# Kernel optimization log

Hardware: AMD Instinct MI355X
Metric: run time of the kernel (lower is better)

## Reference

```python
import jax, jax.numpy as jnp
import numpy as np

WIN = 7
SHIFT = 3
HEADS = 6
EPS = 1e-5


def _rel_pos_index(ws):
    coords = np.stack(np.meshgrid(np.arange(ws), np.arange(ws), indexing='ij')).reshape(2, -1)
    rel = (coords[:, :, None] - coords[:, None, :]).transpose(1, 2, 0)  # (N, N, 2)
    rel[..., 0] += ws - 1
    rel[..., 1] += ws - 1
    rel[..., 0] *= 2 * ws - 1
    return jnp.asarray(rel.sum(-1).reshape(-1))  # (N*N,)


def _attn_mask(H, W, ws, ss):
    img = np.zeros((H, W))
    sl = (slice(0, -ws), slice(-ws, -ss), slice(-ss, None))
    cnt = 0
    for hs in sl:
        for wss in sl:
            img[hs, wss] = cnt
            cnt += 1
    mw = img.reshape(H // ws, ws, W // ws, ws).transpose(0, 2, 1, 3).reshape(-1, ws * ws)
    am = mw[:, None, :] - mw[:, :, None]  # (nw, N, N): mw[j]-mw[i]
    return jnp.asarray(np.where(am != 0, -1e9, 0.0).astype(np.float32))


def _layernorm(x, g, b):
    mu = x.mean(-1, keepdims=True)
    var = ((x - mu) ** 2).mean(-1, keepdims=True)
    return (x - mu) * jax.lax.rsqrt(var + EPS) * g + b


def setup_inputs() -> dict:
    key = jax.random.key(0)
    ks = jax.random.split(key, 6)
    B, H, W, C = 4, 224, 224, 192
    return {
        'x': jax.random.normal(ks[0], (B, H * W, C), jnp.float32),
        'norm1_g': jnp.ones((C,), jnp.float32),
        'norm1_b': jnp.zeros((C,), jnp.float32),
        'qkv_w': jax.random.normal(ks[1], (C, 3 * C), jnp.float32) * 0.02,
        'qkv_b': jnp.zeros((3 * C,), jnp.float32),
        'rpb_table': jax.random.normal(ks[2], ((2 * WIN - 1) ** 2, HEADS), jnp.float32) * 0.02,
        'proj_w': jax.random.normal(ks[3], (C, C), jnp.float32) * 0.02,
        'proj_b': jnp.zeros((C,), jnp.float32),
        'norm2_g': jnp.ones((C,), jnp.float32),
        'norm2_b': jnp.zeros((C,), jnp.float32),
        'fc1_w': jax.random.normal(ks[4], (C, 4 * C), jnp.float32) * 0.02,
        'fc1_b': jnp.zeros((4 * C,), jnp.float32),
        'fc2_w': jax.random.normal(ks[5], (4 * C, C), jnp.float32) * 0.02,
        'fc2_b': jnp.zeros((C,), jnp.float32),
        'h': 224,
        'w': 224,
    }


def reference(x, norm1_g, norm1_b, qkv_w, qkv_b, rpb_table, proj_w, proj_b,
              norm2_g, norm2_b, fc1_w, fc1_b, fc2_w, fc2_b, h, w):
    B, L, C = x.shape
    ch = C // HEADS
    N = WIN * WIN
    nh, nw = h // WIN, w // WIN
    rel_idx = _rel_pos_index(WIN)
    mask = _attn_mask(h, w, WIN, SHIFT)  # (nh*nw, N, N)

    shortcut = x
    xn = _layernorm(x, norm1_g, norm1_b).reshape(B, h, w, C)
    xs = jnp.roll(xn, (-SHIFT, -SHIFT), axis=(1, 2))
    # window partition -> (B*nh*nw, N, C)
    xw = xs.reshape(B, nh, WIN, nw, WIN, C).transpose(0, 1, 3, 2, 4, 5).reshape(B * nh * nw, N, C)

    qkv = (xw @ qkv_w + qkv_b).reshape(-1, N, 3, HEADS, ch).transpose(2, 0, 3, 1, 4)
    q, k, v = qkv[0], qkv[1], qkv[2]  # (NW, HEADS, N, ch)
    scale = ch ** -0.5
    attn = jnp.einsum('whic,whjc->whij', q * scale, k)
    bias = rpb_table[rel_idx].reshape(N, N, HEADS).transpose(2, 0, 1)  # (HEADS, N, N)
    attn = attn + bias[None]
    attn = attn.reshape(B, nh * nw, HEADS, N, N) + mask[None, :, None]
    attn = jax.nn.softmax(attn, axis=-1).reshape(B * nh * nw, HEADS, N, N)

    out = jnp.einsum('whij,whjc->whic', attn, v).transpose(0, 2, 1, 3).reshape(-1, N, C)
    out = out @ proj_w + proj_b
    # window reverse + roll back
    out = out.reshape(B, nh, nw, WIN, WIN, C).transpose(0, 1, 3, 2, 4, 5).reshape(B, h, w, C)
    out = jnp.roll(out, (SHIFT, SHIFT), axis=(1, 2)).reshape(B, L, C)

    x = shortcut + out
    xn2 = _layernorm(x, norm2_g, norm2_b)
    hid = jax.nn.gelu(xn2 @ fc1_w + fc1_b, approximate=False)
    return x + (hid @ fc2_w + fc2_b)
```

## Files before the change

### kernel.cpp

```cpp
#include <hip/hip_runtime.h>
#include <stdint.h>

#define MB    50176
#define WINB  1024
#define CDIM  192

typedef __attribute__((ext_vector_type(8))) short bf16x8;
typedef __attribute__((ext_vector_type(4))) float f32x4;

__device__ __forceinline__ float wsum(float v){
  #pragma unroll
  for (int m=32;m>=1;m>>=1) v += __shfl_xor(v,m,64);
  return v;
}
__device__ __forceinline__ float bfbits2f(uint32_t h){
  union{uint32_t u; float f;} x; x.u = h<<16; return x.f;
}
__device__ __forceinline__ uint16_t f2bfbits(float f){
  union{float ff; uint32_t u;} x; x.ff = f;
  return (uint16_t)((x.u + 0x7FFFu + ((x.u>>16)&1u)) >> 16);
}
__device__ __forceinline__ void gload16(const void* g, void* l){
  __builtin_amdgcn_global_load_lds(
      (const __attribute__((address_space(1))) uint32_t*)g,
      (__attribute__((address_space(3))) uint32_t*)l, 16, 0, 0);
}

__global__ __launch_bounds__(256) void wconv_kernel(
    const float* __restrict__ W, uint16_t* __restrict__ WT, int K, int N){
  int idx = blockIdx.x*256 + threadIdx.x;
  if (idx >= K*N) return;
  int k = idx / N, n = idx - k*N;
  WT[(size_t)n*K + k] = f2bfbits(W[idx]);
}

__global__ __launch_bounds__(256) void btbl_kernel(
    const float* __restrict__ rpb, float* __restrict__ tbl){
  int idx = blockIdx.x*256 + threadIdx.x;
  if (idx >= 4*6*64*64) return;
  int j = idx & 63, i = (idx>>6) & 63;
  int hd = (idx>>12) % 6, cls = idx >> 12; cls /= 6;
  float v = -1e9f;
  if (i < 49 && j < 49){
    int dh = i/7 - j/7, dw = i%7 - j%7;
    v = rpb[((dh+6)*13 + (dw+6))*6 + hd];
    int cH = cls>>1, cW = cls&1;
    int li = (cH ? (i/7 < 4 ? 1 : 2) : 0)*3 + (cW ? (i%7 < 4 ? 1 : 2) : 0);
    int lj = (cH ? (j/7 < 4 ? 1 : 2) : 0)*3 + (cW ? (j%7 < 4 ? 1 : 2) : 0);
    if (li != lj) v = -1e9f;
  }
  tbl[idx] = v;
}

template<bool GATHER>
__global__ __launch_bounds__(256) void ln_kernel(
    const float* __restrict__ src, const float* __restrict__ g,
    const float* __restrict__ bt, uint16_t* __restrict__ dst){
  int wid  = (int)((blockIdx.x*256u + threadIdx.x) >> 6);
  int lane = threadIdx.x & 63;
  int sidx;
  if (GATHER){
    int widx = wid/49, tpos = wid - widx*49;
    int wh = widx>>5, ww = widx&31;
    int th = tpos/7, tw = tpos - th*7;
    int h = wh*7+th+3; if (h>=224) h-=224;
    int w = ww*7+tw+3; if (w>=224) w-=224;
    sidx = h*224 + w;
  } else {
    sidx = wid;
  }
  const float* s = src + (size_t)sidx*CDIM;
  float v0=s[lane], v1=s[lane+64], v2=s[lane+128];
  float mu  = wsum(v0+v1+v2) * (1.f/192.f);
  float var = wsum(v0*v0+v1*v1+v2*v2)*(1.f/192.f) - mu*mu;
  float rs  = rsqrtf(var + 1e-5f);
  uint16_t* d = dst + (size_t)wid*CDIM;
  d[lane]     = f2bfbits((v0-mu)*rs*g[lane]     + bt[lane]);
  d[lane+64]  = f2bfbits((v1-mu)*rs*g[lane+64]  + bt[lane+64]);
  d[lane+128] = f2bfbits((v2-mu)*rs*g[lane+128] + bt[lane+128]);
}

enum { EPI_QKV=0, EPI_PROJ=1, EPI_FC1=2, EPI_FC2=3 };

template<int EPI, int K, int NN>
__global__ __launch_bounds__(256) void mgemm(
    const uint16_t* __restrict__ A, const uint16_t* __restrict__ WT,
    const float* __restrict__ bias, void* __restrict__ outp,
    const float* __restrict__ resid){
  __shared__ __attribute__((aligned(16))) char As[128*128];
  __shared__ __attribute__((aligned(16))) char Bs[64*128];
  const int tid  = threadIdx.x;
  const int lane = tid & 63;
  const int wid  = tid >> 6;
  const int brow = blockIdx.y * 128;
  const int bcol = blockIdx.x * 64;

  f32x4 acc[4][2];
  #pragma unroll
  for (int m=0;m<4;m++)
    #pragma unroll
    for (int n=0;n<2;n++) acc[m][n] = (f32x4){0.f,0.f,0.f,0.f};

  const int srow = lane >> 3;
  const int sg   = (lane & 7) ^ srow;
  const int wm = wid >> 1, wn = wid & 1;
  const int lrow16 = lane & 15, lkh = lane >> 4;

  for (int k0 = 0; k0 < K; k0 += 64){
    #pragma unroll
    for (int c = 0; c < 4; c++){
      int ch = wid*4 + c;
      const uint16_t* g = A + (size_t)(brow + ch*8 + srow)*K + k0 + sg*8;
      gload16(g, As + ch*1024);
    }
    #pragma unroll
    for (int c = 0; c < 2; c++){
      int ch = wid*2 + c;
      const uint16_t* g = WT + (size_t)(bcol + ch*8 + srow)*K + k0 + sg*8;
      gload16(g, Bs + ch*1024);
    }
    __syncthreads();

    bf16x8 af[4][2], bfr[2][2];
    #pragma unroll
    for (int m=0;m<4;m++)
      #pragma unroll
      for (int ks=0;ks<2;ks++){
        int arow = wm*64 + m*16 + lrow16;
        int g0 = ks*4 + lkh;
        af[m][ks] = *(const bf16x8*)(As + arow*128 + ((g0 ^ (arow&7))<<4));
      }
    #pragma unroll
    for (int n=0;n<2;n++)
      #pragma unroll
      for (int ks=0;ks<2;ks++){
        int brn = wn*32 + n*16 + lrow16;
        int g0 = ks*4 + lkh;
        bfr[n][ks] = *(const bf16x8*)(Bs + brn*128 + ((g0 ^ (brn&7))<<4));
      }
    #pragma unroll
    for (int m=0;m<4;m++)
      #pragma unroll
      for (int n=0;n<2;n++)
        #pragma unroll
        for (int ks=0;ks<2;ks++)
          acc[m][n] = __builtin_amdgcn_mfma_f32_16x16x32_bf16(
              af[m][ks], bfr[n][ks], acc[m][n], 0, 0, 0);
    __syncthreads();
  }

  float bi[2];
  #pragma unroll
  for (int n=0;n<2;n++) bi[n] = bias[bcol + wn*32 + n*16 + lrow16];
  #pragma unroll
  for (int m=0;m<4;m++){
    #pragma unroll
    for (int j=0;j<4;j++){
      int r = brow + wm*64 + m*16 + lkh*4 + j;
      if constexpr (EPI==EPI_QKV || EPI==EPI_FC1){
        #pragma unroll
        for (int n=0;n<2;n++){
          float v = acc[m][n][j] + bi[n];
          if constexpr (EPI==EPI_FC1)
            v = 0.5f*v*(1.f + erff(v*0.70710678118654752f));
          ((uint16_t*)outp)[(size_t)r*NN + bcol + wn*32 + n*16 + lrow16] = f2bfbits(v);
        }
      } else if constexpr (EPI==EPI_PROJ){
        int widx = r/49, tpos = r - widx*49;
        int wh = widx>>5, ww = widx&31;
        int th = tpos/7, tw = tpos - th*7;
        int h = wh*7+th+3; if (h>=224) h-=224;
        int w = ww*7+tw+3; if (w>=224) w-=224;
        size_t pr = ((size_t)h*224 + w)*CDIM;
        #pragma unroll
        for (int n=0;n<2;n++){
          size_t p = pr + bcol + wn*32 + n*16 + lrow16;
          ((float*)outp)[p] = acc[m][n][j] + bi[n] + resid[p];
        }
      } else {
        size_t pr = (size_t)r*NN;
        #pragma unroll
        for (int n=0;n<2;n++){
          size_t p = pr + bcol + wn*32 + n*16 + lrow16;
          ((float*)outp)[p] = acc[m][n][j] + bi[n] + resid[p];
        }
      }
    }
  }
}

__global__ __launch_bounds__(64) void attn_kernel(
    const uint16_t* __restrict__ qkv, const float* __restrict__ btbl,
    uint16_t* __restrict__ attnout){
  const int bid  = blockIdx.x;
  const int widx = bid/6, hd = bid - widx*6;
  const int lane = threadIdx.x;
  const int r16 = lane & 15, t4 = lane >> 4;
  __shared__ uint16_t Vt[32][72];
  __shared__ uint16_t Pl[4][16][72];

  #pragma unroll
  for (int e=lane; e<32*16; e+=64){ Vt[e>>4][48 + (e&15)] = 0; }
  for (int ch = lane; ch < 196; ch += 64){
    int j = ch >> 2, c0 = (ch&3)*8;
    const uint16_t* src = qkv + ((size_t)widx*49 + j)*576 + hd*32 + 384 + c0;
    uint4 v = *(const uint4*)src;
    uint32_t u[4] = {v.x, v.y, v.z, v.w};
    #pragma unroll
    for (int q=0;q<8;q++) Vt[c0+q][j] = (uint16_t)(u[q>>1] >> ((q&1)*16));
  }

  bf16x8 kf[4], qf[4];
  #pragma unroll
  for (int jt=0;jt<4;jt++)
    kf[jt] = *(const bf16x8*)(qkv + ((size_t)widx*49 + jt*16 + r16)*576 + hd*32 + 192 + t4*8);
  #pragma unroll
  for (int it=0;it<4;it++)
    qf[it] = *(const bf16x8*)(qkv + ((size_t)widx*49 + it*16 + r16)*576 + hd*32 + t4*8);
  f32x4 acc[4][4];
  #pragma unroll
  for (int jt=0;jt<4;jt++)
    #pragma unroll
    for (int it=0;it<4;it++){
      acc[jt][it] = (f32x4){0.f,0.f,0.f,0.f};
      acc[jt][it] = __builtin_amdgcn_mfma_f32_16x16x32_bf16(kf[jt], qf[it], acc[jt][it], 0,0,0);
    }

  const int wh = widx>>5, ww = widx&31;
  const int cls = ((wh==31)<<1) | (ww==31);
  const float* tb = btbl + ((size_t)(cls*6 + hd) << 12);
  const float scale = 0.17677669529663689f;
  #pragma unroll
  for (int it=0;it<4;it++){
    int i = it*16 + r16;
    float s[4][4];
    float m = -3.4e38f;
    #pragma unroll
    for (int jt=0;jt<4;jt++){
      float4 bv = *(const float4*)(tb + i*64 + jt*16 + t4*4);
      float bb[4] = {bv.x, bv.y, bv.z, bv.w};
      #pragma unroll
      for (int r=0;r<4;r++){
        s[jt][r] = acc[jt][it][r]*scale + bb[r];
        m = fmaxf(m, s[jt][r]);
      }
    }
    m = fmaxf(m, __shfl_xor(m, 16, 64));
    m = fmaxf(m, __shfl_xor(m, 32, 64));
    float sum = 0.f;
    #pragma unroll
    for (int jt=0;jt<4;jt++)
      #pragma unroll
      for (int r=0;r<4;r++){
        s[jt][r] = __expf(s[jt][r] - m);
        sum += s[jt][r];
      }
    sum += __shfl_xor(sum, 16, 64);
    sum += __shfl_xor(sum, 32, 64);
    float inv = 1.f / sum;
    #pragma unroll
    for (int jt=0;jt<4;jt++){
      uint32_t lo = (uint32_t)f2bfbits(s[jt][0]*inv) | ((uint32_t)f2bfbits(s[jt][1]*inv) << 16);
      uint32_t hi = (uint32_t)f2bfbits(s[jt][2]*inv) | ((uint32_t)f2bfbits(s[jt][3]*inv) << 16);
      *(uint2*)&Pl[it][r16][jt*16 + t4*4] = make_uint2(lo, hi);
    }
  }
  __syncthreads();

  bf16x8 bv[2][2];
  #pragma unroll
  for (int ct=0;ct<2;ct++)
    #pragma unroll
    for (int ks=0;ks<2;ks++)
      bv[ct][ks] = *(const bf16x8*)&Vt[ct*16 + r16][ks*32 + t4*8];
  #pragma unroll
  for (int it=0;it<4;it++){
    f32x4 o[2];
    o[0] = (f32x4){0.f,0.f,0.f,0.f};
    o[1] = (f32x4){0.f,0.f,0.f,0.f};
    #pragma unroll
    for (int ks=0;ks<2;ks++){
      bf16x8 pa = *(const bf16x8*)&Pl[it][r16][ks*32 + t4*8];
      #pragma unroll
      for (int ct=0;ct<2;ct++)
        o[ct] = __builtin_amdgcn_mfma_f32_16x16x32_bf16(pa, bv[ct][ks], o[ct], 0,0,0);
    }
    #pragma unroll
    for (int r=0;r<4;r++){
      int i = it*16 + t4*4 + r;
      if (i < 49){
        size_t base = ((size_t)widx*49 + i)*CDIM + hd*32;
        attnout[base + r16]      = f2bfbits(o[0][r]);
        attnout[base + 16 + r16] = f2bfbits(o[1][r]);
      }
    }
  }
}

extern "C" void kernel_launch(void* const* d_in, const int* in_sizes, int n_in,
                              void* d_out, int out_size, void* d_ws, size_t ws_size,
                              hipStream_t stream) {
  const float* x       = (const float*)d_in[0];
  const float* n1g     = (const float*)d_in[1];
  const float* n1b     = (const float*)d_in[2];
  const float* qkv_w   = (const float*)d_in[3];
  const float* qkv_b   = (const float*)d_in[4];
  const float* rpb     = (const float*)d_in[5];
  const float* proj_w  = (const float*)d_in[6];
  const float* proj_b  = (const float*)d_in[7];
  const float* n2g     = (const float*)d_in[8];
  const float* n2b     = (const float*)d_in[9];
  const float* fc1_w   = (const float*)d_in[10];
  const float* fc1_b   = (const float*)d_in[11];
  const float* fc2_w   = (const float*)d_in[12];
  const float* fc2_b   = (const float*)d_in[13];
  float* out = (float*)d_out;

  char* ws = (char*)d_ws;
  uint16_t* Abuf = (uint16_t*)ws;
  uint16_t* Bq   = (uint16_t*)(ws + (size_t)MB*CDIM*2);
  char*     wbase = ws + (size_t)MB*CDIM*2 + (size_t)MB*768*2;
  uint16_t* qkvW = (uint16_t*)wbase;
  uint16_t* prjW = (uint16_t*)(wbase + 221184);
  uint16_t* fc1W = (uint16_t*)(wbase + 221184 + 73728);
  uint16_t* fc2W = (uint16_t*)(wbase + 221184 + 73728 + 294912);
  float*    btbl = (float*)(wbase + 221184 + 73728 + 294912 + 294912);

  wconv_kernel<<<(192*576+255)/256, 256, 0, stream>>>(qkv_w,  qkvW, 192, 576);
  wconv_kernel<<<(192*192+255)/256, 256, 0, stream>>>(proj_w, prjW, 192, 192);
  wconv_kernel<<<(192*768+255)/256, 256, 0, stream>>>(fc1_w,  fc1W, 192, 768);
  wconv_kernel<<<(768*192+255)/256, 256, 0, stream>>>(fc2_w,  fc2W, 768, 192);
  btbl_kernel<<<(4*6*64*64+255)/256, 256, 0, stream>>>(rpb, btbl);

  for (int b=0;b<4;b++){
    const float* xb = x   + (size_t)b*MB*CDIM;
    float*      ob  = out + (size_t)b*MB*CDIM;
    ln_kernel<true><<<MB/4, 256, 0, stream>>>(xb, n1g, n1b, Abuf);
    mgemm<EPI_QKV, 192, 576>
        <<<dim3(9, MB/128), 256, 0, stream>>>(Abuf, qkvW, qkv_b, (void*)Bq, nullptr);
    attn_kernel<<<WINB*6, 64, 0, stream>>>(Bq, btbl, Abuf);
    mgemm<EPI_PROJ, 192, 192>
        <<<dim3(3, MB/128), 256, 0, stream>>>(Abuf, prjW, proj_b, (void*)ob, xb);
  }
  for (int b=0;b<4;b++){
    float* ob = out + (size_t)b*MB*CDIM;
    ln_kernel<false><<<MB/4, 256, 0, stream>>>(ob, n2g, n2b, Abuf);
    mgemm<EPI_FC1, 192, 768>
        <<<dim3(12, MB/128), 256, 0, stream>>>(Abuf, fc1W, fc1_b, (void*)Bq, nullptr);
    mgemm<EPI_FC2, 768, 192>
        <<<dim3(3, MB/128), 256, 0, stream>>>(Bq, fc2W, fc2_b, (void*)ob, ob);
  }
}
```

Before: 835.0 us.

## Fuse projection with LayerNorm2, batch all images per launch, merge prep kernels

```diff
diff --git a/kernel.cpp b/kernel.cpp
--- a/kernel.cpp
+++ b/kernel.cpp
@@ -2,7 +2,6 @@
 #include <stdint.h>
 
 #define MB    50176
-#define WINB  1024
 #define CDIM  192
 
 typedef __attribute__((ext_vector_type(8))) short bf16x8;
@@ -25,21 +24,33 @@
       (const __attribute__((address_space(1))) uint32_t*)g,
       (__attribute__((address_space(3))) uint32_t*)l, 16, 0, 0);
 }
-
-__global__ __launch_bounds__(256) void wconv_kernel(
-    const float* __restrict__ W, uint16_t* __restrict__ WT, int K, int N){
+__device__ __forceinline__ size_t row2tok(int r_g){
+  int widx = r_g/49, tpos = r_g - widx*49;
+  int b = widx>>10, rem = widx&1023;
+  int h = (rem>>5)*7 + tpos/7 + 3; if (h>=224) h-=224;
+  int w = (rem&31)*7 + (tpos - (tpos/7)*7) + 3; if (w>=224) w-=224;
+  return (size_t)b*MB + (size_t)h*224 + w;
+}
+
+__global__ __launch_bounds__(256) void prep_kernel(
+    const float* __restrict__ qkv_w, const float* __restrict__ proj_w,
+    const float* __restrict__ fc1_w, const float* __restrict__ fc2_w,
+    const float* __restrict__ rpb,
+    uint16_t* __restrict__ qkvW, uint16_t* __restrict__ prjW,
+    uint16_t* __restrict__ fc1W, uint16_t* __restrict__ fc2W,
+    float* __restrict__ btbl){
   int idx = blockIdx.x*256 + threadIdx.x;
-  if (idx >= K*N) return;
-  int k = idx / N, n = idx - k*N;
-  WT[(size_t)n*K + k] = f2bfbits(W[idx]);
-}
-
-__global__ __launch_bounds__(256) void btbl_kernel(
-    const float* __restrict__ rpb, float* __restrict__ tbl){
-  int idx = blockIdx.x*256 + threadIdx.x;
-  if (idx >= 4*6*64*64) return;
+  if (idx < 110592){ int k=idx/576, n=idx-k*576; qkvW[n*192+k]=f2bfbits(qkv_w[idx]); return; }
+  idx -= 110592;
+  if (idx < 36864){ int k=idx/192, n=idx-k*192; prjW[n*192+k]=f2bfbits(proj_w[idx]); return; }
+  idx -= 36864;
+  if (idx < 147456){ int k=idx/768, n=idx-k*768; fc1W[n*192+k]=f2bfbits(fc1_w[idx]); return; }
+  idx -= 147456;
+  if (idx < 147456){ int k=idx/192, n=idx-k*192; fc2W[n*768+k]=f2bfbits(fc2_w[idx]); return; }
+  idx -= 147456;
+  if (idx >= 98304) return;
   int j = idx & 63, i = (idx>>6) & 63;
-  int hd = (idx>>12) % 6, cls = idx >> 12; cls /= 6;
+  int hd = (idx>>12) % 6, cls = (idx>>12)/6;
   float v = -1e9f;
   if (i < 49 && j < 49){
     int dh = i/7 - j/7, dw = i%7 - j%7;
@@ -49,44 +60,33 @@
     int lj = (cH ? (j/7 < 4 ? 1 : 2) : 0)*3 + (cW ? (j%7 < 4 ? 1 : 2) : 0);
     if (li != lj) v = -1e9f;
   }
-  tbl[idx] = v;
-}
-
-template<bool GATHER>
-__global__ __launch_bounds__(256) void ln_kernel(
-    const float* __restrict__ src, const float* __restrict__ g,
-    const float* __restrict__ bt, uint16_t* __restrict__ dst){
-  int wid  = (int)((blockIdx.x*256u + threadIdx.x) >> 6);
-  int lane = threadIdx.x & 63;
-  int sidx;
-  if (GATHER){
-    int widx = wid/49, tpos = wid - widx*49;
-    int wh = widx>>5, ww = widx&31;
-    int th = tpos/7, tw = tpos - th*7;
-    int h = wh*7+th+3; if (h>=224) h-=224;
-    int w = ww*7+tw+3; if (w>=224) w-=224;
-    sidx = h*224 + w;
-  } else {
-    sidx = wid;
-  }
-  const float* s = src + (size_t)sidx*CDIM;
+  btbl[idx] = v;
+}
+
+__global__ __launch_bounds__(256) void ln1_kernel(
+    const float* __restrict__ x, const float* __restrict__ g,
+    const float* __restrict__ bt, uint16_t* __restrict__ dst, int row0){
+  int wid_l = (int)((blockIdx.x*256u + threadIdx.x) >> 6);
+  int lane  = threadIdx.x & 63;
+  size_t sidx = row2tok(row0 + wid_l);
+  const float* s = x + sidx*CDIM;
   float v0=s[lane], v1=s[lane+64], v2=s[lane+128];
   float mu  = wsum(v0+v1+v2) * (1.f/192.f);
   float var = wsum(v0*v0+v1*v1+v2*v2)*(1.f/192.f) - mu*mu;
   float rs  = rsqrtf(var + 1e-5f);
-  uint16_t* d = dst + (size_t)wid*CDIM;
+  uint16_t* d = dst + (size_t)wid_l*CDIM;
   d[lane]     = f2bfbits((v0-mu)*rs*g[lane]     + bt[lane]);
   d[lane+64]  = f2bfbits((v1-mu)*rs*g[lane+64]  + bt[lane+64]);
   d[lane+128] = f2bfbits((v2-mu)*rs*g[lane+128] + bt[lane+128]);
 }
 
-enum { EPI_QKV=0, EPI_PROJ=1, EPI_FC1=2, EPI_FC2=3 };
+enum { EPI_QKV=0, EPI_FC1=2, EPI_FC2=3 };
 
 template<int EPI, int K, int NN>
 __global__ __launch_bounds__(256) void mgemm(
     const uint16_t* __restrict__ A, const uint16_t* __restrict__ WT,
     const float* __restrict__ bias, void* __restrict__ outp,
-    const float* __restrict__ resid){
+    const float* __restrict__ resid, int row0){
   __shared__ __attribute__((aligned(16))) char As[128*128];
   __shared__ __attribute__((aligned(16))) char Bs[64*128];
   const int tid  = threadIdx.x;
@@ -110,14 +110,12 @@
     #pragma unroll
     for (int c = 0; c < 4; c++){
       int ch = wid*4 + c;
-      const uint16_t* g = A + (size_t)(brow + ch*8 + srow)*K + k0 + sg*8;
-      gload16(g, As + ch*1024);
+      gload16(A + (size_t)(brow + ch*8 + srow)*K + k0 + sg*8, As + ch*1024);
     }
     #pragma unroll
     for (int c = 0; c < 2; c++){
       int ch = wid*2 + c;
-      const uint16_t* g = WT + (size_t)(bcol + ch*8 + srow)*K + k0 + sg*8;
-      gload16(g, Bs + ch*1024);
+      gload16(WT + (size_t)(bcol + ch*8 + srow)*K + k0 + sg*8, Bs + ch*1024);
     }
     __syncthreads();
 
@@ -127,16 +125,14 @@
       #pragma unroll
       for (int ks=0;ks<2;ks++){
         int arow = wm*64 + m*16 + lrow16;
-        int g0 = ks*4 + lkh;
-        af[m][ks] = *(const bf16x8*)(As + arow*128 + ((g0 ^ (arow&7))<<4));
+        af[m][ks] = *(const bf16x8*)(As + arow*128 + (((ks*4+lkh) ^ (arow&7))<<4));
       }
     #pragma unroll
     for (int n=0;n<2;n++)
       #pragma unroll
       for (int ks=0;ks<2;ks++){
         int brn = wn*32 + n*16 + lrow16;
-        int g0 = ks*4 + lkh;
-        bfr[n][ks] = *(const bf16x8*)(Bs + brn*128 + ((g0 ^ (brn&7))<<4));
+        bfr[n][ks] = *(const bf16x8*)(Bs + brn*128 + (((ks*4+lkh) ^ (brn&7))<<4));
       }
     #pragma unroll
     for (int m=0;m<4;m++)
@@ -165,25 +161,120 @@
             v = 0.5f*v*(1.f + erff(v*0.70710678118654752f));
           ((uint16_t*)outp)[(size_t)r*NN + bcol + wn*32 + n*16 + lrow16] = f2bfbits(v);
         }
-      } else if constexpr (EPI==EPI_PROJ){
-        int widx = r/49, tpos = r - widx*49;
-        int wh = widx>>5, ww = widx&31;
-        int th = tpos/7, tw = tpos - th*7;
-        int h = wh*7+th+3; if (h>=224) h-=224;
-        int w = ww*7+tw+3; if (w>=224) w-=224;
-        size_t pr = ((size_t)h*224 + w)*CDIM;
+      } else {
+        size_t pr = row2tok(row0 + r)*CDIM;
         #pragma unroll
         for (int n=0;n<2;n++){
           size_t p = pr + bcol + wn*32 + n*16 + lrow16;
           ((float*)outp)[p] = acc[m][n][j] + bi[n] + resid[p];
         }
-      } else {
-        size_t pr = (size_t)r*NN;
+      }
+    }
+  }
+}
+
+__global__ __launch_bounds__(384) void proj_ln2(
+    const uint16_t* __restrict__ A, const uint16_t* __restrict__ WT,
+    const float* __restrict__ pbias, const float* __restrict__ x,
+    const float* __restrict__ g2, const float* __restrict__ b2,
+    float* __restrict__ xout, uint16_t* __restrict__ ln2out, int row0){
+  __shared__ __attribute__((aligned(16))) char As[128*128];
+  __shared__ __attribute__((aligned(16))) char Bs[192*128];
+  __shared__ float stats[3][128][2];
+  const int tid  = threadIdx.x;
+  const int lane = tid & 63;
+  const int wid  = tid >> 6;
+  const int wm = wid >> 2, wn3 = wid & 3;
+  const int pm = wid / 3, pn = wid - pm*3;
+  const int brow = blockIdx.x * 128;
+  const int srow = lane >> 3;
+  const int sg   = (lane & 7) ^ srow;
+  const int lrow16 = lane & 15, lkh = lane >> 4;
+  (void)wm; (void)wn3;
+
+  f32x4 acc[4][4];
+  #pragma unroll
+  for (int m=0;m<4;m++)
+    #pragma unroll
+    for (int n=0;n<4;n++) acc[m][n] = (f32x4){0.f,0.f,0.f,0.f};
+
+  for (int k0 = 0; k0 < 192; k0 += 64){
+    for (int ch = wid; ch < 16; ch += 6)
+      gload16(A + (size_t)(brow + ch*8 + srow)*192 + k0 + sg*8, As + ch*1024);
+    for (int ch = wid; ch < 24; ch += 6)
+      gload16(WT + (size_t)(ch*8 + srow)*192 + k0 + sg*8, Bs + ch*1024);
+    __syncthreads();
+
+    bf16x8 af[4][2], bfr[4][2];
+    #pragma unroll
+    for (int m=0;m<4;m++)
+      #pragma unroll
+      for (int ks=0;ks<2;ks++){
+        int arow = pm*64 + m*16 + lrow16;
+        af[m][ks] = *(const bf16x8*)(As + arow*128 + (((ks*4+lkh) ^ (arow&7))<<4));
+      }
+    #pragma unroll
+    for (int n=0;n<4;n++)
+      #pragma unroll
+      for (int ks=0;ks<2;ks++){
+        int brn = pn*64 + n*16 + lrow16;
+        bfr[n][ks] = *(const bf16x8*)(Bs + brn*128 + (((ks*4+lkh) ^ (brn&7))<<4));
+      }
+    #pragma unroll
+    for (int m=0;m<4;m++)
+      #pragma unroll
+      for (int n=0;n<4;n++)
         #pragma unroll
-        for (int n=0;n<2;n++){
-          size_t p = pr + bcol + wn*32 + n*16 + lrow16;
-          ((float*)outp)[p] = acc[m][n][j] + bi[n] + resid[p];
-        }
+        for (int ks=0;ks<2;ks++)
+          acc[m][n] = __builtin_amdgcn_mfma_f32_16x16x32_bf16(
+              af[m][ks], bfr[n][ks], acc[m][n], 0, 0, 0);
+    __syncthreads();
+  }
+
+  float bi[4], g2v[4], b2v[4];
+  #pragma unroll
+  for (int n=0;n<4;n++){
+    int c = pn*64 + n*16 + lrow16;
+    bi[n] = pbias[c]; g2v[n] = g2[c]; b2v[n] = b2[c];
+  }
+  #pragma unroll
+  for (int m=0;m<4;m++){
+    #pragma unroll
+    for (int j=0;j<4;j++){
+      int r = pm*64 + m*16 + lkh*4 + j;
+      size_t pr = row2tok(row0 + brow + r)*CDIM;
+      float s1 = 0.f, s2 = 0.f;
+      #pragma unroll
+      for (int n=0;n<4;n++){
+        int c = pn*64 + n*16 + lrow16;
+        float y = acc[m][n][j] + bi[n] + x[pr + c];
+        acc[m][n][j] = y;
+        xout[pr + c] = y;
+        s1 += y; s2 = fmaf(y, y, s2);
+      }
+      #pragma unroll
+      for (int mk=1; mk<16; mk<<=1){
+        s1 += __shfl_xor(s1, mk, 64);
+        s2 += __shfl_xor(s2, mk, 64);
+      }
+      if (lrow16 == 0){ stats[pn][r][0] = s1; stats[pn][r][1] = s2; }
+    }
+  }
+  __syncthreads();
+  #pragma unroll
+  for (int m=0;m<4;m++){
+    #pragma unroll
+    for (int j=0;j<4;j++){
+      int r = pm*64 + m*16 + lkh*4 + j;
+      float s1 = stats[0][r][0] + stats[1][r][0] + stats[2][r][0];
+      float s2 = stats[0][r][1] + stats[1][r][1] + stats[2][r][1];
+      float mu = s1*(1.f/192.f);
+      float rs = rsqrtf(s2*(1.f/192.f) - mu*mu + 1e-5f);
+      size_t pr = (size_t)(brow + r)*CDIM;
+      #pragma unroll
+      for (int n=0;n<4;n++){
+        int c = pn*64 + n*16 + lrow16;
+        ln2out[pr + c] = f2bfbits((acc[m][n][j]-mu)*rs*g2v[n] + b2v[n]);
       }
     }
   }
@@ -191,13 +282,13 @@
 
 __global__ __launch_bounds__(64) void attn_kernel(
     const uint16_t* __restrict__ qkv, const float* __restrict__ btbl,
-    uint16_t* __restrict__ attnout){
+    uint16_t* __restrict__ attnout, int win0){
   const int bid  = blockIdx.x;
   const int widx = bid/6, hd = bid - widx*6;
   const int lane = threadIdx.x;
   const int r16 = lane & 15, t4 = lane >> 4;
   __shared__ uint16_t Vt[32][72];
-  __shared__ uint16_t Pl[4][16][72];
+  __shared__ uint16_t Pl[16][72];
 
   #pragma unroll
   for (int e=lane; e<32*16; e+=64){ Vt[e>>4][48 + (e&15)] = 0; }
@@ -225,11 +316,20 @@
       acc[jt][it] = (f32x4){0.f,0.f,0.f,0.f};
       acc[jt][it] = __builtin_amdgcn_mfma_f32_16x16x32_bf16(kf[jt], qf[it], acc[jt][it], 0,0,0);
     }
-
-  const int wh = widx>>5, ww = widx&31;
-  const int cls = ((wh==31)<<1) | (ww==31);
+  __syncthreads();
+
+  const int gw = win0 + widx;
+  const int cls = ((((gw&1023)>>5)==31)<<1) | ((gw&31)==31);
   const float* tb = btbl + ((size_t)(cls*6 + hd) << 12);
   const float scale = 0.17677669529663689f;
+
+  bf16x8 bv[2][2];
+  #pragma unroll
+  for (int ct=0;ct<2;ct++)
+    #pragma unroll
+    for (int ks=0;ks<2;ks++)
+      bv[ct][ks] = *(const bf16x8*)&Vt[ct*16 + r16][ks*32 + t4*8];
+
   #pragma unroll
   for (int it=0;it<4;it++){
     int i = it*16 + r16;
@@ -237,8 +337,8 @@
     float m = -3.4e38f;
     #pragma unroll
     for (int jt=0;jt<4;jt++){
-      float4 bv = *(const float4*)(tb + i*64 + jt*16 + t4*4);
-      float bb[4] = {bv.x, bv.y, bv.z, bv.w};
+      float4 bvv = *(const float4*)(tb + i*64 + jt*16 + t4*4);
+      float bb[4] = {bvv.x, bvv.y, bvv.z, bvv.w};
       #pragma unroll
       for (int r=0;r<4;r++){
         s[jt][r] = acc[jt][it][r]*scale + bb[r];
@@ -262,34 +362,25 @@
     for (int jt=0;jt<4;jt++){
       uint32_t lo = (uint32_t)f2bfbits(s[jt][0]*inv) | ((uint32_t)f2bfbits(s[jt][1]*inv) << 16);
       uint32_t hi = (uint32_t)f2bfbits(s[jt][2]*inv) | ((uint32_t)f2bfbits(s[jt][3]*inv) << 16);
-      *(uint2*)&Pl[it][r16][jt*16 + t4*4] = make_uint2(lo, hi);
-    }
-  }
-  __syncthreads();
-
-  bf16x8 bv[2][2];
-  #pragma unroll
-  for (int ct=0;ct<2;ct++)
-    #pragma unroll
-    for (int ks=0;ks<2;ks++)
-      bv[ct][ks] = *(const bf16x8*)&Vt[ct*16 + r16][ks*32 + t4*8];
-  #pragma unroll
-  for (int it=0;it<4;it++){
+      *(uint2*)&Pl[r16][jt*16 + t4*4] = make_uint2(lo, hi);
+    }
+    __syncthreads();
+
     f32x4 o[2];
     o[0] = (f32x4){0.f,0.f,0.f,0.f};
     o[1] = (f32x4){0.f,0.f,0.f,0.f};
     #pragma unroll
     for (int ks=0;ks<2;ks++){
-      bf16x8 pa = *(const bf16x8*)&Pl[it][r16][ks*32 + t4*8];
+      bf16x8 pa = *(const bf16x8*)&Pl[r16][ks*32 + t4*8];
       #pragma unroll
       for (int ct=0;ct<2;ct++)
         o[ct] = __builtin_amdgcn_mfma_f32_16x16x32_bf16(pa, bv[ct][ks], o[ct], 0,0,0);
     }
     #pragma unroll
     for (int r=0;r<4;r++){
-      int i = it*16 + t4*4 + r;
-      if (i < 49){
-        size_t base = ((size_t)widx*49 + i)*CDIM + hd*32;
+      int i2 = it*16 + t4*4 + r;
+      if (i2 < 49){
+        size_t base = ((size_t)widx*49 + i2)*CDIM + hd*32;
         attnout[base + r16]      = f2bfbits(o[0][r]);
         attnout[base + 16 + r16] = f2bfbits(o[1][r]);
       }
@@ -316,38 +407,37 @@
   const float* fc2_b   = (const float*)d_in[13];
   float* out = (float*)d_out;
 
+  const size_t TBL = 221184 + 73728 + 294912 + 294912 + 393216;
+  size_t need_full = (size_t)200704*CDIM*2 + (size_t)200704*768*2 + TBL;
+  bool full = ws_size >= need_full;
+  int T  = full ? 200704 : MB;
+  int NC = full ? 1 : 4;
+  int NW = T / 49;
+
   char* ws = (char*)d_ws;
   uint16_t* Abuf = (uint16_t*)ws;
-  uint16_t* Bq   = (uint16_t*)(ws + (size_t)MB*CDIM*2);
-  char*     wbase = ws + (size_t)MB*CDIM*2 + (size_t)MB*768*2;
+  uint16_t* Bq   = (uint16_t*)(ws + (size_t)T*CDIM*2);
+  char* wbase    = ws + (size_t)T*CDIM*2 + (size_t)T*768*2;
   uint16_t* qkvW = (uint16_t*)wbase;
   uint16_t* prjW = (uint16_t*)(wbase + 221184);
   uint16_t* fc1W = (uint16_t*)(wbase + 221184 + 73728);
   uint16_t* fc2W = (uint16_t*)(wbase + 221184 + 73728 + 294912);
   float*    btbl = (float*)(wbase + 221184 + 73728 + 294912 + 294912);
 
-  wconv_kernel<<<(192*576+255)/256, 256, 0, stream>>>(qkv_w,  qkvW, 192, 576);
-  wconv_kernel<<<(192*192+255)/256, 256, 0, stream>>>(proj_w, prjW, 192, 192);
-  wconv_kernel<<<(192*768+255)/256, 256, 0, stream>>>(fc1_w,  fc1W, 192, 768);
-  wconv_kernel<<<(768*192+255)/256, 256, 0, stream>>>(fc2_w,  fc2W, 768, 192);
-  btbl_kernel<<<(4*6*64*64+255)/256, 256, 0, stream>>>(rpb, btbl);
-
-  for (int b=0;b<4;b++){
-    const float* xb = x   + (size_t)b*MB*CDIM;
-    float*      ob  = out + (size_t)b*MB*CDIM;
-    ln_kernel<true><<<MB/4, 256, 0, stream>>>(xb, n1g, n1b, Abuf);
+  prep_kernel<<<2112, 256, 0, stream>>>(qkv_w, proj_w, fc1_w, fc2_w, rpb,
+                                        qkvW, prjW, fc1W, fc2W, btbl);
+
+  for (int c = 0; c < NC; c++){
+    int row0 = c*T, win0 = row0/49;
+    ln1_kernel<<<T/4, 256, 0, stream>>>(x, n1g, n1b, Abuf, row0);
     mgemm<EPI_QKV, 192, 576>
-        <<<dim3(9, MB/128), 256, 0, stream>>>(Abuf, qkvW, qkv_b, (void*)Bq, nullptr);
-    attn_kernel<<<WINB*6, 64, 0, stream>>>(Bq, btbl, Abuf);
-    mgemm<EPI_PROJ, 192, 192>
-        <<<dim3(3, MB/128), 256, 0, stream>>>(Abuf, prjW, proj_b, (void*)ob, xb);
-  }
-  for (int b=0;b<4;b++){
-    float* ob = out + (size_t)b*MB*CDIM;
-    ln_kernel<false><<<MB/4, 256, 0, stream>>>(ob, n2g, n2b, Abuf);
+        <<<dim3(9, T/128), 256, 0, stream>>>(Abuf, qkvW, qkv_b, (void*)Bq, nullptr, 0);
+    attn_kernel<<<NW*6, 64, 0, stream>>>(Bq, btbl, Abuf, win0);
+    proj_ln2<<<T/128, 384, 0, stream>>>(Abuf, prjW, proj_b, x, n2g, n2b,
+                                        out, Abuf, row0);
     mgemm<EPI_FC1, 192, 768>
-        <<<dim3(12, MB/128), 256, 0, stream>>>(Abuf, fc1W, fc1_b, (void*)Bq, nullptr);
+        <<<dim3(12, T/128), 256, 0, stream>>>(Abuf, fc1W, fc1_b, (void*)Bq, nullptr, 0);
     mgemm<EPI_FC2, 768, 192>
-        <<<dim3(3, MB/128), 256, 0, stream>>>(Bq, fc2W, fc2_b, (void*)ob, ob);
-  }
-}
+        <<<dim3(3, T/128), 256, 0, stream>>>(Bq, fc2W, fc2_b, (void*)out, out, row0);
+  }
+}
```

Result: faster. 798.3 us (-4.4%).
